# Performance work log

Measured on AMD Instinct MI355X. Metric: run time of the kernel, lower is better.

## Reference

```python
import jax, jax.numpy as jnp
import numpy as np

D_MODEL = 1024
N_HEADS = 16
HEAD_DIM = D_MODEL // N_HEADS
D_FF = 4096
ROPE_BASE = 10000.0
LN_EPS = 1e-5


def setup_inputs() -> dict:
    key = jax.random.key(0)
    ks = jax.random.split(key, 12)
    B, S = 2, 2048
    s = 0.02
    inp = {
        "x": jax.random.normal(ks[0], (B, S, D_MODEL), dtype=jnp.float32),
        "Wq": jax.random.normal(ks[1], (D_MODEL, D_MODEL), dtype=jnp.float32) * s,
        "bq": jnp.zeros((D_MODEL,), jnp.float32),
        "Wk": jax.random.normal(ks[2], (D_MODEL, D_MODEL), dtype=jnp.float32) * s,
        "bk": jnp.zeros((D_MODEL,), jnp.float32),
        "Wv": jax.random.normal(ks[3], (D_MODEL, D_MODEL), dtype=jnp.float32) * s,
        "bv": jnp.zeros((D_MODEL,), jnp.float32),
        "Wo": jax.random.normal(ks[4], (D_MODEL, D_MODEL), dtype=jnp.float32) * s,
        "bo": jnp.zeros((D_MODEL,), jnp.float32),
        "ln1_g": jnp.ones((D_MODEL,), jnp.float32),
        "ln1_b": jnp.zeros((D_MODEL,), jnp.float32),
        "W1": jax.random.normal(ks[5], (D_MODEL, D_FF), dtype=jnp.float32) * s,
        "b1": jnp.zeros((D_FF,), jnp.float32),
        "W2": jax.random.normal(ks[6], (D_FF, D_MODEL), dtype=jnp.float32) * s,
        "b2": jnp.zeros((D_MODEL,), jnp.float32),
        "ln2_g": jnp.ones((D_MODEL,), jnp.float32),
        "ln2_b": jnp.zeros((D_MODEL,), jnp.float32),
    }
    return inp


def _layernorm(x, g, b):
    mu = jnp.mean(x, axis=-1, keepdims=True)
    var = jnp.var(x, axis=-1, keepdims=True)
    return (x - mu) * jax.lax.rsqrt(var + LN_EPS) * g + b


def _rope_cos_sin(seq_len, dtype):
    inv_freq = 1.0 / (ROPE_BASE ** (jnp.arange(0, HEAD_DIM, 2, dtype=jnp.float32) / HEAD_DIM))
    t = jnp.arange(seq_len, dtype=jnp.float32)
    freqs = jnp.einsum("i,j->ij", t, inv_freq)          # [S, HEAD_DIM/2]
    emb = jnp.concatenate([freqs, freqs], axis=-1)        # [S, HEAD_DIM]
    return jnp.cos(emb).astype(dtype), jnp.sin(emb).astype(dtype)


def _rotate_half(x):
    x1, x2 = jnp.split(x, 2, axis=-1)
    return jnp.concatenate([-x2, x1], axis=-1)


def reference(x, Wq, bq, Wk, bk, Wv, bv, Wo, bo, ln1_g, ln1_b,
              W1, b1, W2, b2, ln2_g, ln2_b):
    B, S, _ = x.shape
    residual = x
    h = _layernorm(x, ln1_g, ln1_b)

    def split_heads(y):  # [B,S,D] -> [B,H,S,hd]
        return y.reshape(B, S, N_HEADS, HEAD_DIM).transpose(0, 2, 1, 3)

    q = split_heads(h @ Wq + bq)
    k = split_heads(h @ Wk + bk)
    v = split_heads(h @ Wv + bv)

    cos, sin = _rope_cos_sin(S, x.dtype)  # [S, hd], broadcast over B,H
    q = q * cos + _rotate_half(q) * sin
    k = k * cos + _rotate_half(k) * sin

    scale = HEAD_DIM ** -0.5
    scores = jnp.einsum("bhqd,bhkd->bhqk", q, k) * scale
    attn = jax.nn.softmax(scores, axis=-1)
    ctx = jnp.einsum("bhqk,bhkd->bhqd", attn, v)           # [B,H,S,hd]
    ctx = ctx.transpose(0, 2, 1, 3).reshape(B, S, D_MODEL)
    attn_out = ctx @ Wo + bo

    x = residual + attn_out
    residual = x
    h = _layernorm(x, ln2_g, ln2_b)
    ffn = jax.nn.gelu(h @ W1 + b1, approximate=False) @ W2 + b2
    return residual + ffn
```

## Files before the change

kernel.cpp:

```cpp
#include <hip/hip_runtime.h>
#include <hip/hip_bf16.h>
#include <stdint.h>

#define S_LEN 2048
#define NH 16
#define HD 64
#define DM 1024
#define DFF 4096
#define MTOK 4096

typedef __attribute__((ext_vector_type(8))) short short8;
typedef __attribute__((ext_vector_type(4))) float f32x4;
typedef unsigned short u16;
typedef unsigned int u32;

__device__ __forceinline__ float bf2f(u16 u) {
  union { u32 i; float f; } x; x.i = ((u32)u) << 16; return x.f;
}
__device__ __forceinline__ u16 f2bf(float f) {
  union { float f; u32 i; } x; x.f = f;
  u32 r = x.i + 0x7fffu + ((x.i >> 16) & 1u);
  return (u16)(r >> 16);
}
__device__ __forceinline__ void gload16(const u16* g, u16* l) {
  __builtin_amdgcn_global_load_lds(
      (__attribute__((address_space(1))) u32*)g,
      (__attribute__((address_space(3))) u32*)l, 16, 0, 0);
}

#define VM0 asm volatile("s_waitcnt vmcnt(0)" ::: "memory")
#define VM6 asm volatile("s_waitcnt vmcnt(6)" ::: "memory")
#define BARR do { __builtin_amdgcn_s_barrier(); asm volatile("" ::: "memory"); } while (0)
#define LGKM0 do { asm volatile("s_waitcnt lgkmcnt(0)" ::: "memory"); __builtin_amdgcn_sched_barrier(0); } while (0)
#define PRIO1 __builtin_amdgcn_s_setprio(1)
#define PRIO0 __builtin_amdgcn_s_setprio(0)

__device__ __forceinline__ void transpose_tile(const float* __restrict__ W,
                                               u16* __restrict__ Wt, int K, int N,
                                               int n0, int k0, int tx, int ty,
                                               float (*tile)[33]) {
#pragma unroll
  for (int i = 0; i < 4; ++i)
    tile[ty + i * 8][tx] = W[(size_t)(k0 + ty + i * 8) * N + n0 + tx];
  __syncthreads();
#pragma unroll
  for (int i = 0; i < 4; ++i)
    Wt[(size_t)(n0 + ty + i * 8) * K + k0 + tx] = f2bf(tile[tx][ty + i * 8]);
}

__global__ __launch_bounds__(256) void prep(
    const float* __restrict__ Wq, const float* __restrict__ Wk,
    const float* __restrict__ Wv, const float* __restrict__ Wo,
    const float* __restrict__ W1, const float* __restrict__ W2,
    u16* __restrict__ WQKVT, u16* __restrict__ WOT, u16* __restrict__ W1T,
    u16* __restrict__ W2T, float* __restrict__ cosT, float* __restrict__ sinT,
    const float* __restrict__ x, const float* __restrict__ g,
    const float* __restrict__ b, u16* __restrict__ H) {
  __shared__ float tile[32][33];
  __shared__ float red[8];
  const int r = blockIdx.x;
  const int t = threadIdx.x;
  const int tx = t & 31, ty = t >> 5;
  if (r < 4096) {
    const float* W = (r < 1024) ? Wq : (r < 2048) ? Wk : (r < 3072) ? Wv : Wo;
    u16* Wt = (r < 1024) ? WQKVT
              : (r < 2048) ? WQKVT + 1024 * 1024
              : (r < 3072) ? WQKVT + 2 * 1024 * 1024 : WOT;
    int sub = r & 1023;
    transpose_tile(W, Wt, 1024, 1024, (sub & 31) * 32, (sub >> 5) * 32, tx, ty, tile);
  } else if (r < 8192) {
    int sub = r - 4096;
    transpose_tile(W1, W1T, 1024, 4096, (sub & 127) * 32, (sub >> 7) * 32, tx, ty, tile);
  } else if (r < 12288) {
    int sub = r - 8192;
    transpose_tile(W2, W2T, 4096, 1024, (sub & 31) * 32, (sub >> 5) * 32, tx, ty, tile);
  } else if (r < 12544) {
    int id = (r - 12288) * 256 + t;
    int s = id >> 5, j = id & 31;
    float inv = powf(10000.0f, -(float)j * (1.0f / 32.0f));
    float fr = (float)s * inv;
    cosT[id] = cosf(fr);
    sinT[id] = sinf(fr);
  } else {
    int row = r - 12544;
    float4 v = ((const float4*)(x + ((size_t)row << 10)))[t];
    float s = v.x + v.y + v.z + v.w;
    float q = v.x * v.x + v.y * v.y + v.z * v.z + v.w * v.w;
#pragma unroll
    for (int m = 1; m < 64; m <<= 1) {
      s += __shfl_xor(s, m, 64);
      q += __shfl_xor(q, m, 64);
    }
    int lane = t & 63, w = t >> 6;
    if (lane == 0) { red[w] = s; red[4 + w] = q; }
    __syncthreads();
    s = red[0] + red[1] + red[2] + red[3];
    q = red[4] + red[5] + red[6] + red[7];
    float mu = s * (1.0f / 1024.0f);
    float var = q * (1.0f / 1024.0f) - mu * mu;
    float rstd = rsqrtf(var + 1e-5f);
    float4 gv = ((const float4*)g)[t];
    float4 bv = ((const float4*)b)[t];
    ushort4 o;
    o.x = f2bf((v.x - mu) * rstd * gv.x + bv.x);
    o.y = f2bf((v.y - mu) * rstd * gv.y + bv.y);
    o.z = f2bf((v.z - mu) * rstd * gv.z + bv.z);
    o.w = f2bf((v.w - mu) * rstd * gv.w + bv.w);
    ((ushort4*)(H + ((size_t)row << 10)))[t] = o;
  }
}

__global__ __launch_bounds__(256) void ln_bf16(const float* __restrict__ x,
                                               const float* __restrict__ g,
                                               const float* __restrict__ b,
                                               u16* __restrict__ out) {
  int row = blockIdx.x;
  int t = threadIdx.x;
  float4 v = ((const float4*)(x + ((size_t)row << 10)))[t];
  float s = v.x + v.y + v.z + v.w;
  float q = v.x * v.x + v.y * v.y + v.z * v.z + v.w * v.w;
#pragma unroll
  for (int m = 1; m < 64; m <<= 1) {
    s += __shfl_xor(s, m, 64);
    q += __shfl_xor(q, m, 64);
  }
  __shared__ float red[8];
  int lane = t & 63, w = t >> 6;
  if (lane == 0) { red[w] = s; red[4 + w] = q; }
  __syncthreads();
  s = red[0] + red[1] + red[2] + red[3];
  q = red[4] + red[5] + red[6] + red[7];
  float mu = s * (1.0f / 1024.0f);
  float var = q * (1.0f / 1024.0f) - mu * mu;
  float rstd = rsqrtf(var + 1e-5f);
  float4 gv = ((const float4*)g)[t];
  float4 bv = ((const float4*)b)[t];
  ushort4 o;
  o.x = f2bf((v.x - mu) * rstd * gv.x + bv.x);
  o.y = f2bf((v.y - mu) * rstd * gv.y + bv.y);
  o.z = f2bf((v.z - mu) * rstd * gv.z + bv.z);
  o.w = f2bf((v.w - mu) * rstd * gv.w + bv.w);
  ((ushort4*)(out + ((size_t)row << 10)))[t] = o;
}

#define MMQ(IB, NB)                                                          \
  _Pragma("unroll") for (int i_ = 0; i_ < 4; ++i_)                           \
  _Pragma("unroll") for (int n_ = 0; n_ < 2; ++n_)                           \
  _Pragma("unroll") for (int k_ = 0; k_ < 2; ++k_)                           \
    acc[(IB) + i_][(NB) + n_] = __builtin_amdgcn_mfma_f32_16x16x32_bf16(     \
        a[i_][k_], b[(NB) + n_][k_], acc[(IB) + i_][(NB) + n_], 0, 0, 0);

template <int EPI>
__global__ __launch_bounds__(512, 2) void gemm256(
    const u16* __restrict__ A, const u16* __restrict__ Bt, int N, int K,
    const float* __restrict__ bias, const float* __restrict__ bq,
    const float* __restrict__ bk, const float* __restrict__ bv,
    const float* __restrict__ cosT, const float* __restrict__ sinT,
    u16* __restrict__ d0, u16* __restrict__ d1, u16* __restrict__ d2) {
  __shared__ __align__(16) u16 As[2][256 * 64];
  __shared__ __align__(16) u16 Bs[2][256 * 64];
  const int t = threadIdx.x;
  const int lane = t & 63, wid = t >> 6;
  const int fr = lane & 15, fq = lane >> 4;
  const int m0 = blockIdx.y << 8, n0 = blockIdx.x << 8;
  const int wmo = (wid >> 2) << 7;
  const int wno = (wid & 3) << 6;
  const int r7 = fr & 7;
  const int srow = t >> 3, ssl = t & 7;

  f32x4 acc[8][4];
#pragma unroll
  for (int i = 0; i < 8; ++i)
#pragma unroll
    for (int n = 0; n < 4; ++n) acc[i][n] = (f32x4){0.f, 0.f, 0.f, 0.f};

  short8 a[4][2], b[4][2];

  auto stageA = [&](int slot, int kt) {
#pragma unroll
    for (int c = 0; c < 4; ++c) {
      const int row = (c << 6) + srow;
      gload16(A + (size_t)(m0 + row) * K + kt + ((ssl ^ (row & 7)) << 3),
              &As[slot][(size_t)((c << 9) + t) << 3]);
    }
  };
  auto stageB = [&](int slot, int kt) {
#pragma unroll
    for (int c = 0; c < 4; ++c) {
      const int row = (c << 6) + srow;
      gload16(Bt + (size_t)(n0 + row) * K + kt + ((ssl ^ (row & 7)) << 3),
              &Bs[slot][(size_t)((c << 9) + t) << 3]);
    }
  };
  auto readA = [&](int slot, int ibase) {
#pragma unroll
    for (int i = 0; i < 4; ++i) {
      const u16* rp = &As[slot][(wmo + ((ibase + i) << 4) + fr) << 6];
      a[i][0] = *(const short8*)(rp + ((fq ^ r7) << 3));
      a[i][1] = *(const short8*)(rp + (((4 + fq) ^ r7) << 3));
    }
  };
  auto readB = [&](int slot, int nbase) {
#pragma unroll
    for (int n = 0; n < 2; ++n) {
      const u16* rp = &Bs[slot][(wno + ((nbase + n) << 4) + fr) << 6];
      b[nbase + n][0] = *(const short8*)(rp + ((fq ^ r7) << 3));
      b[nbase + n][1] = *(const short8*)(rp + (((4 + fq) ^ r7) << 3));
    }
  };

  stageA(0, 0);
  stageB(0, 0);
  const int iters = K >> 7;
  for (int it = 0; it < iters; ++it) {
    const int kt = it << 7;
    VM0; BARR;
    readA(0, 0); readB(0, 0);
    stageA(1, kt + 64);
    LGKM0; PRIO1; MMQ(0, 0); PRIO0;
    BARR;
    readB(0, 2);
    stageB(1, kt + 64);
    LGKM0; PRIO1; MMQ(0, 2); PRIO0;
    BARR;
    readA(0, 4);
    LGKM0; PRIO1; MMQ(4, 2); PRIO0;
    BARR;
    PRIO1; MMQ(4, 0); PRIO0;
    VM0; BARR;
    readA(1, 0); readB(1, 0);
    if (it + 1 < iters) stageA(0, kt + 128);
    LGKM0; PRIO1; MMQ(0, 0); PRIO0;
    BARR;
    readB(1, 2);
    if (it + 1 < iters) stageB(0, kt + 128);
    LGKM0; PRIO1; MMQ(0, 2); PRIO0;
    BARR;
    readA(1, 4);
    LGKM0; PRIO1; MMQ(4, 2); PRIO0;
    BARR;
    PRIO1; MMQ(4, 0); PRIO0;
  }

  if (EPI == 0) {
    const int colbase = n0 + wno;
    const int slice = colbase >> 10;
    const int cb = colbase & 1023;
    const int hh = cb >> 6;
    if (slice < 2) {
      const float sc = (slice == 0) ? 0.125f * 1.44269504088896f : 1.0f;
      const float* bb_ = (slice == 0) ? bq : bk;
      u16* dst = (slice == 0) ? d0 : d1;
#pragma unroll
      for (int i = 0; i < 8; ++i) {
        const int row0 = m0 + wmo + (i << 4) + (fq << 2);
#pragma unroll
        for (int n = 0; n < 2; ++n) {
          const int d = n * 16 + fr;
          const float blo = bb_[cb + d];
          const float bhi = bb_[cb + d + 32];
#pragma unroll
          for (int j = 0; j < 4; ++j) {
            const int row = row0 + j;
            const int ss = row & 2047, bb2 = row >> 11;
            const float c = cosT[ss * 32 + d];
            const float sn = sinT[ss * 32 + d];
            const float av = acc[i][n][j] + blo;
            const float bv2 = acc[i][n + 2][j] + bhi;
            const size_t base = ((size_t)((bb2 * 16 + hh) * 2048 + ss)) << 6;
            dst[base + d] = f2bf((av * c - bv2 * sn) * sc);
            dst[base + d + 32] = f2bf((bv2 * c + av * sn) * sc);
          }
        }
      }
    } else {
#pragma unroll
      for (int i = 0; i < 8; ++i) {
        const int row0 = m0 + wmo + (i << 4) + (fq << 2);
#pragma unroll
        for (int n = 0; n < 4; ++n) {
          const int d = n * 16 + fr;
          const float bia = bv[cb + d];
#pragma unroll
          for (int j = 0; j < 4; ++j) {
            const int row = row0 + j;
            const int ss = row & 2047, bb2 = row >> 11;
            d2[((size_t)((bb2 * 16 + hh) * 64 + d)) * 2048 + ss] =
                f2bf(acc[i][n][j] + bia);
          }
        }
      }
    }
  } else {
#pragma unroll
    for (int i = 0; i < 8; ++i) {
      const int row0 = m0 + wmo + (i << 4) + (fq << 2);
#pragma unroll
      for (int n = 0; n < 4; ++n) {
        const int col = n0 + wno + n * 16 + fr;
        const float bia = bias[col];
#pragma unroll
        for (int j = 0; j < 4; ++j) {
          const int row = row0 + j;
          const float v = acc[i][n][j] + bia;
          const float gl = 0.5f * v * (1.0f + erff(v * 0.70710678118f));
          d0[(size_t)row * N + col] = f2bf(gl);
        }
      }
    }
  }
}

__global__ __launch_bounds__(256, 2) void gemm_bt2(
    const u16* __restrict__ A, const u16* __restrict__ Bt, int K,
    const float* __restrict__ bias, const float* __restrict__ resid,
    float* __restrict__ dst) {
  __shared__ __align__(16) u16 As[3][128 * 64];
  __shared__ __align__(16) u16 Bs[3][64 * 64];
  const int t = threadIdx.x, lane = t & 63, wid = t >> 6;
  const int fr = lane & 15, fq = lane >> 4;
  const int bid = blockIdx.x;
  const int xcd = bid & 7, within = bid >> 3;
  const int m0 = (xcd * 4 + (within >> 4)) << 7;
  const int n0 = (within & 15) << 6;
  const int wm = (wid >> 1) << 6;
  const int wn = (wid & 1) << 5;
  const int sr = t >> 3, sl = t & 7;
  const int sw7 = fr & 7;

  f32x4 acc[4][2];
#pragma unroll
  for (int i = 0; i < 4; ++i)
#pragma unroll
    for (int n = 0; n < 2; ++n) acc[i][n] = (f32x4){0.f, 0.f, 0.f, 0.f};

  auto stage = [&](int b, int kt) {
#pragma unroll
    for (int c = 0; c < 4; ++c) {
      int R = c * 32 + sr;
      gload16(A + (size_t)(m0 + R) * K + kt + ((sl ^ (R & 7)) << 3),
              &As[b][R * 64 + sl * 8]);
    }
#pragma unroll
    for (int c = 0; c < 2; ++c) {
      int R = c * 32 + sr;
      gload16(Bt + (size_t)(n0 + R) * K + kt + ((sl ^ (R & 7)) << 3),
              &Bs[b][R * 64 + sl * 8]);
    }
  };

  stage(0, 0);
  stage(1, 64);
  const int iters = K >> 6;
  for (int it = 0; it < iters; ++it) {
    if (it + 1 < iters) { VM6; } else { VM0; }
    BARR;
    if (it + 2 < iters) stage((it + 2) % 3, (it + 2) << 6);
    const int slot = it % 3;
    short8 a[4][2], b[2][2];
#pragma unroll
    for (int i = 0; i < 4; ++i) {
      const char* rp = (const char*)&As[slot][(wm + i * 16 + fr) * 64];
      a[i][0] = *(const short8*)(rp + ((fq ^ sw7) << 4));
      a[i][1] = *(const short8*)(rp + (((4 + fq) ^ sw7) << 4));
    }
#pragma unroll
    for (int n = 0; n < 2; ++n) {
      const char* rp = (const char*)&Bs[slot][(wn + n * 16 + fr) * 64];
      b[n][0] = *(const short8*)(rp + ((fq ^ sw7) << 4));
      b[n][1] = *(const short8*)(rp + (((4 + fq) ^ sw7) << 4));
    }
    PRIO1;
#pragma unroll
    for (int i = 0; i < 4; ++i)
#pragma unroll
      for (int n = 0; n < 2; ++n)
#pragma unroll
        for (int k2 = 0; k2 < 2; ++k2)
          acc[i][n] = __builtin_amdgcn_mfma_f32_16x16x32_bf16(a[i][k2], b[n][k2],
                                                              acc[i][n], 0, 0, 0);
    PRIO0;
  }

#pragma unroll
  for (int i = 0; i < 4; ++i) {
    int row0 = m0 + wm + i * 16 + (fq << 2);
#pragma unroll
    for (int n = 0; n < 2; ++n) {
      int col = n0 + wn + n * 16 + fr;
      float bia = bias[col];
#pragma unroll
      for (int j = 0; j < 4; ++j) {
        size_t idx = (size_t)(row0 + j) * 1024 + col;
        dst[idx] = acc[i][n][j] + bia + resid[idx];
      }
    }
  }
}

__global__ __launch_bounds__(256, 4) void attn_fwd(const u16* __restrict__ q,
                                                   const u16* __restrict__ k,
                                                   const u16* __restrict__ vt,
                                                   u16* __restrict__ ctx) {
  __shared__ __align__(16) u16 Ks[2][64 * 64];
  __shared__ __align__(16) u16 Vs[2][64 * 64];
  __shared__ __align__(16) u16 Pb[4][16 * 64];
  const int t = threadIdx.x, lane = t & 63, w = t >> 6;
  const int fr = lane & 15, fq = lane >> 4;
  const int bid = blockIdx.x;
  const int bh = (bid & 7) * 4 + ((bid >> 3) & 3);
  const int qt = bid >> 5;
  const int q0w = qt * 64 + w * 16;
  const size_t hbase = (size_t)bh << 17;
  const u16* kg = k + hbase;
  const u16* vg = vt + hbase;
  const int sr = t >> 3;
  const int sl = t & 7;
  const int sw7 = fr & 7;

  short8 aq0, aq1;
  {
    const u16* qp = q + hbase + (size_t)(q0w + fr) * 64 + fq * 8;
    aq0 = *(const short8*)qp;
    aq1 = *(const short8*)(qp + 32);
  }

  float mrow = -3e38f, lrow = 0.f;
  f32x4 o[4];
#pragma unroll
  for (int n = 0; n < 4; ++n) o[n] = (f32x4){0.f, 0.f, 0.f, 0.f};

  auto stage = [&](int buf, int kt) {
#pragma unroll
    for (int c = 0; c < 2; ++c) {
      int R = c * 32 + sr;
      int gs = sl ^ (R & 7);
      gload16(kg + (size_t)(kt + R) * 64 + gs * 8, &Ks[buf][R * 64 + sl * 8]);
    }
#pragma unroll
    for (int c = 0; c < 2; ++c) {
      int R = c * 32 + sr;
      int gs = sl ^ (R & 7);
      gload16(vg + (size_t)R * 2048 + kt + gs * 8, &Vs[buf][R * 64 + sl * 8]);
    }
  };

  stage(0, 0);
  int buf = 0;
  for (int it = 0; it < 32; ++it) {
    VM0;
    BARR;
    if (it < 31) stage(buf ^ 1, (it + 1) * 64);

    f32x4 s[4];
    const char* kbase = (const char*)&Ks[buf][0];
    PRIO1;
#pragma unroll
    for (int n = 0; n < 4; ++n) {
      const char* kr = kbase + (n * 16 + fr) * 128;
      short8 kb0 = *(const short8*)(kr + ((fq ^ sw7) << 4));
      short8 kb1 = *(const short8*)(kr + (((4 + fq) ^ sw7) << 4));
      s[n] = (f32x4){0.f, 0.f, 0.f, 0.f};
      s[n] = __builtin_amdgcn_mfma_f32_16x16x32_bf16(kb0, aq0, s[n], 0, 0, 0);
      s[n] = __builtin_amdgcn_mfma_f32_16x16x32_bf16(kb1, aq1, s[n], 0, 0, 0);
    }
    PRIO0;

    float m0 = fmaxf(fmaxf(s[0][0], s[0][1]), fmaxf(s[0][2], s[0][3]));
    float m1 = fmaxf(fmaxf(s[1][0], s[1][1]), fmaxf(s[1][2], s[1][3]));
    float m2 = fmaxf(fmaxf(s[2][0], s[2][1]), fmaxf(s[2][2], s[2][3]));
    float m3 = fmaxf(fmaxf(s[3][0], s[3][1]), fmaxf(s[3][2], s[3][3]));
    float pm = fmaxf(fmaxf(m0, m1), fmaxf(m2, m3));
    pm = fmaxf(pm, __shfl_xor(pm, 16, 64));
    pm = fmaxf(pm, __shfl_xor(pm, 32, 64));

    if (!__all(pm - mrow <= 8.0f)) {
      float mnew = fmaxf(mrow, pm);
      float alpha = exp2f(mrow - mnew);
      mrow = mnew;
      lrow *= alpha;
      float al[4];
#pragma unroll
      for (int j = 0; j < 4; ++j) al[j] = __shfl(alpha, fq * 4 + j, 64);
#pragma unroll
      for (int n = 0; n < 4; ++n)
#pragma unroll
        for (int j = 0; j < 4; ++j) o[n][j] *= al[j];
    }

    float rs = 0.f;
    char* pw = (char*)&Pb[w][0];
#pragma unroll
    for (int n = 0; n < 4; ++n) {
#pragma unroll
      for (int jp = 0; jp < 2; ++jp) {
        float p0 = exp2f(s[n][2 * jp] - mrow);
        float p1 = exp2f(s[n][2 * jp + 1] - mrow);
        rs += p0 + p1;
        union { float f; u32 i; } u0, u1;
        u0.f = p0; u1.f = p1;
        u32 pk = (u0.i >> 16) | (u1.i & 0xffff0000u);
        int off = fr * 128 + ((n * 32 + fq * 8 + jp * 4) ^ (sw7 << 4));
        *(u32*)(pw + off) = pk;
      }
    }
    rs += __shfl_xor(rs, 16, 64);
    rs += __shfl_xor(rs, 32, 64);
    lrow += rs;

    LGKM0;
    const char* prd = (const char*)&Pb[w][0];
    short8 ap0 = *(const short8*)(prd + fr * 128 + ((fq ^ sw7) << 4));
    short8 ap1 = *(const short8*)(prd + fr * 128 + (((4 + fq) ^ sw7) << 4));

    const char* vbase = (const char*)&Vs[buf][0];
    PRIO1;
#pragma unroll
    for (int n = 0; n < 4; ++n) {
      const char* vr = vbase + (n * 16 + fr) * 128;
      short8 vb0 = *(const short8*)(vr + ((fq ^ sw7) << 4));
      short8 vb1 = *(const short8*)(vr + (((4 + fq) ^ sw7) << 4));
      o[n] = __builtin_amdgcn_mfma_f32_16x16x32_bf16(ap0, vb0, o[n], 0, 0, 0);
      o[n] = __builtin_amdgcn_mfma_f32_16x16x32_bf16(ap1, vb1, o[n], 0, 0, 0);
    }
    PRIO0;
    buf ^= 1;
  }

  const int bb = bh >> 4, hh = bh & 15;
  float rl[4];
#pragma unroll
  for (int j = 0; j < 4; ++j) rl[j] = 1.0f / __shfl(lrow, fq * 4 + j, 64);
#pragma unroll
  for (int n = 0; n < 4; ++n) {
    int d = n * 16 + fr;
#pragma unroll
    for (int j = 0; j < 4; ++j) {
      int row = q0w + fq * 4 + j;
      ctx[(((size_t)(bb * 2048 + row)) << 10) + hh * 64 + d] = f2bf(o[n][j] * rl[j]);
    }
  }
}

extern "C" void kernel_launch(void* const* d_in, const int* in_sizes, int n_in,
                              void* d_out, int out_size, void* d_ws, size_t ws_size,
                              hipStream_t stream) {
  const float* x    = (const float*)d_in[0];
  const float* Wq   = (const float*)d_in[1];
  const float* bq   = (const float*)d_in[2];
  const float* Wk   = (const float*)d_in[3];
  const float* bk   = (const float*)d_in[4];
  const float* Wv   = (const float*)d_in[5];
  const float* bv   = (const float*)d_in[6];
  const float* Wo   = (const float*)d_in[7];
  const float* bo   = (const float*)d_in[8];
  const float* ln1g = (const float*)d_in[9];
  const float* ln1b = (const float*)d_in[10];
  const float* W1   = (const float*)d_in[11];
  const float* b1   = (const float*)d_in[12];
  const float* W2   = (const float*)d_in[13];
  const float* b2   = (const float*)d_in[14];
  const float* ln2g = (const float*)d_in[15];
  const float* ln2b = (const float*)d_in[16];

  char* ws = (char*)d_ws;
  size_t off = 0;
  auto alloc = [&](size_t bytes) {
    char* p = ws + off;
    off += (bytes + 1023) & ~(size_t)1023;
    return p;
  };
  u16* WQKVT = (u16*)alloc((size_t)3 * DM * DM * 2);
  u16* WOT = (u16*)alloc((size_t)DM * DM * 2);
  u16* W1T = (u16*)alloc((size_t)DFF * DM * 2);
  u16* W2T = (u16*)alloc((size_t)DM * DFF * 2);
  float* COS = (float*)alloc((size_t)S_LEN * 32 * 4);
  float* SIN = (float*)alloc((size_t)S_LEN * 32 * 4);
  u16* H   = (u16*)alloc((size_t)MTOK * DM * 2);
  u16* Qb  = (u16*)alloc((size_t)MTOK * DM * 2);
  u16* Kb  = (u16*)alloc((size_t)MTOK * DM * 2);
  u16* VT  = (u16*)alloc((size_t)MTOK * DM * 2);
  u16* CTX = (u16*)alloc((size_t)MTOK * DM * 2);
  float* X2 = (float*)alloc((size_t)MTOK * DM * 4);
  u16* FFN1 = Qb;
  if (ws_size < off) return;

  dim3 blk256(256);
  prep<<<dim3(16640), blk256, 0, stream>>>(Wq, Wk, Wv, Wo, W1, W2, WQKVT, WOT,
                                           W1T, W2T, COS, SIN, x, ln1g, ln1b, H);
  gemm256<0><<<dim3(12, 16), dim3(512), 0, stream>>>(
      H, WQKVT, 3072, 1024, nullptr, bq, bk, bv, COS, SIN, Qb, Kb, VT);
  attn_fwd<<<dim3(1024), blk256, 0, stream>>>(Qb, Kb, VT, CTX);
  gemm_bt2<<<dim3(512), blk256, 0, stream>>>(CTX, WOT, 1024, bo, x, X2);
  ln_bf16<<<4096, blk256, 0, stream>>>(X2, ln2g, ln2b, H);
  gemm256<1><<<dim3(16, 16), dim3(512), 0, stream>>>(
      H, W1T, 4096, 1024, b1, nullptr, nullptr, nullptr, nullptr, nullptr,
      FFN1, nullptr, nullptr);
  gemm_bt2<<<dim3(512), blk256, 0, stream>>>(FFN1, W2T, 4096, b2, X2, (float*)d_out);
}
```

Measured before the change: 260.1 us.

## Process two query fragments per wave in attention to reuse K/V tiles

Each wave in the attention kernel now handles 32 query rows (two 16-row fragments) instead of 16. Each block covers 128 queries, so the grid halves. K and V fragments read from LDS are reused across both query fragments, which halves K/V global staging and LDS reads per query. P is packed with the v_cvt_pk_bf16_f32 instruction and written as 8-byte stores. The cost is more registers (launch bounds lowered from 4 to 2 blocks per SM), fewer blocks (512) and therefore less occupancy, and conversion switches from truncation to round-to-nearest.

```diff
diff --git a/kernel.cpp b/kernel.cpp
--- a/kernel.cpp
+++ b/kernel.cpp
@@ -398,19 +398,19 @@
   }
 }
 
-__global__ __launch_bounds__(256, 4) void attn_fwd(const u16* __restrict__ q,
+__global__ __launch_bounds__(256, 2) void attn_fwd(const u16* __restrict__ q,
                                                    const u16* __restrict__ k,
                                                    const u16* __restrict__ vt,
                                                    u16* __restrict__ ctx) {
   __shared__ __align__(16) u16 Ks[2][64 * 64];
   __shared__ __align__(16) u16 Vs[2][64 * 64];
-  __shared__ __align__(16) u16 Pb[4][16 * 64];
+  __shared__ __align__(16) u16 Pb[4][2][16 * 64];
   const int t = threadIdx.x, lane = t & 63, w = t >> 6;
   const int fr = lane & 15, fq = lane >> 4;
   const int bid = blockIdx.x;
   const int bh = (bid & 7) * 4 + ((bid >> 3) & 3);
   const int qt = bid >> 5;
-  const int q0w = qt * 64 + w * 16;
+  const int q0w = qt * 128 + w * 32;
   const size_t hbase = (size_t)bh << 17;
   const u16* kg = k + hbase;
   const u16* vg = vt + hbase;
@@ -418,17 +418,20 @@
   const int sl = t & 7;
   const int sw7 = fr & 7;
 
-  short8 aq0, aq1;
-  {
-    const u16* qp = q + hbase + (size_t)(q0w + fr) * 64 + fq * 8;
-    aq0 = *(const short8*)qp;
-    aq1 = *(const short8*)(qp + 32);
-  }
-
-  float mrow = -3e38f, lrow = 0.f;
-  f32x4 o[4];
-#pragma unroll
-  for (int n = 0; n < 4; ++n) o[n] = (f32x4){0.f, 0.f, 0.f, 0.f};
+  short8 aq[2][2];
+#pragma unroll
+  for (int qf = 0; qf < 2; ++qf) {
+    const u16* qp = q + hbase + (size_t)(q0w + qf * 16 + fr) * 64 + fq * 8;
+    aq[qf][0] = *(const short8*)qp;
+    aq[qf][1] = *(const short8*)(qp + 32);
+  }
+
+  float mrow[2] = {-3e38f, -3e38f}, lrow[2] = {0.f, 0.f};
+  f32x4 o[2][4];
+#pragma unroll
+  for (int qf = 0; qf < 2; ++qf)
+#pragma unroll
+    for (int n = 0; n < 4; ++n) o[qf][n] = (f32x4){0.f, 0.f, 0.f, 0.f};
 
   auto stage = [&](int buf, int kt) {
 #pragma unroll
@@ -452,66 +455,86 @@
     BARR;
     if (it < 31) stage(buf ^ 1, (it + 1) * 64);
 
-    f32x4 s[4];
+    short8 kb[4][2];
     const char* kbase = (const char*)&Ks[buf][0];
-    PRIO1;
 #pragma unroll
     for (int n = 0; n < 4; ++n) {
       const char* kr = kbase + (n * 16 + fr) * 128;
-      short8 kb0 = *(const short8*)(kr + ((fq ^ sw7) << 4));
-      short8 kb1 = *(const short8*)(kr + (((4 + fq) ^ sw7) << 4));
-      s[n] = (f32x4){0.f, 0.f, 0.f, 0.f};
-      s[n] = __builtin_amdgcn_mfma_f32_16x16x32_bf16(kb0, aq0, s[n], 0, 0, 0);
-      s[n] = __builtin_amdgcn_mfma_f32_16x16x32_bf16(kb1, aq1, s[n], 0, 0, 0);
-    }
+      kb[n][0] = *(const short8*)(kr + ((fq ^ sw7) << 4));
+      kb[n][1] = *(const short8*)(kr + (((4 + fq) ^ sw7) << 4));
+    }
+    f32x4 s[2][4];
+    PRIO1;
+#pragma unroll
+    for (int qf = 0; qf < 2; ++qf)
+#pragma unroll
+      for (int n = 0; n < 4; ++n) {
+        s[qf][n] = (f32x4){0.f, 0.f, 0.f, 0.f};
+        s[qf][n] = __builtin_amdgcn_mfma_f32_16x16x32_bf16(kb[n][0], aq[qf][0], s[qf][n], 0, 0, 0);
+        s[qf][n] = __builtin_amdgcn_mfma_f32_16x16x32_bf16(kb[n][1], aq[qf][1], s[qf][n], 0, 0, 0);
+      }
     PRIO0;
 
-    float m0 = fmaxf(fmaxf(s[0][0], s[0][1]), fmaxf(s[0][2], s[0][3]));
-    float m1 = fmaxf(fmaxf(s[1][0], s[1][1]), fmaxf(s[1][2], s[1][3]));
-    float m2 = fmaxf(fmaxf(s[2][0], s[2][1]), fmaxf(s[2][2], s[2][3]));
-    float m3 = fmaxf(fmaxf(s[3][0], s[3][1]), fmaxf(s[3][2], s[3][3]));
-    float pm = fmaxf(fmaxf(m0, m1), fmaxf(m2, m3));
-    pm = fmaxf(pm, __shfl_xor(pm, 16, 64));
-    pm = fmaxf(pm, __shfl_xor(pm, 32, 64));
-
-    if (!__all(pm - mrow <= 8.0f)) {
-      float mnew = fmaxf(mrow, pm);
-      float alpha = exp2f(mrow - mnew);
-      mrow = mnew;
-      lrow *= alpha;
-      float al[4];
-#pragma unroll
-      for (int j = 0; j < 4; ++j) al[j] = __shfl(alpha, fq * 4 + j, 64);
-#pragma unroll
-      for (int n = 0; n < 4; ++n)
-#pragma unroll
-        for (int j = 0; j < 4; ++j) o[n][j] *= al[j];
-    }
-
-    float rs = 0.f;
-    char* pw = (char*)&Pb[w][0];
-#pragma unroll
-    for (int n = 0; n < 4; ++n) {
-#pragma unroll
-      for (int jp = 0; jp < 2; ++jp) {
-        float p0 = exp2f(s[n][2 * jp] - mrow);
-        float p1 = exp2f(s[n][2 * jp + 1] - mrow);
-        rs += p0 + p1;
-        union { float f; u32 i; } u0, u1;
-        u0.f = p0; u1.f = p1;
-        u32 pk = (u0.i >> 16) | (u1.i & 0xffff0000u);
-        int off = fr * 128 + ((n * 32 + fq * 8 + jp * 4) ^ (sw7 << 4));
-        *(u32*)(pw + off) = pk;
-      }
-    }
-    rs += __shfl_xor(rs, 16, 64);
-    rs += __shfl_xor(rs, 32, 64);
-    lrow += rs;
+    float pm[2];
+#pragma unroll
+    for (int qf = 0; qf < 2; ++qf) {
+      float a0 = fmaxf(fmaxf(s[qf][0][0], s[qf][0][1]), fmaxf(s[qf][0][2], s[qf][0][3]));
+      float a1 = fmaxf(fmaxf(s[qf][1][0], s[qf][1][1]), fmaxf(s[qf][1][2], s[qf][1][3]));
+      float a2 = fmaxf(fmaxf(s[qf][2][0], s[qf][2][1]), fmaxf(s[qf][2][2], s[qf][2][3]));
+      float a3 = fmaxf(fmaxf(s[qf][3][0], s[qf][3][1]), fmaxf(s[qf][3][2], s[qf][3][3]));
+      float m = fmaxf(fmaxf(a0, a1), fmaxf(a2, a3));
+      m = fmaxf(m, __shfl_xor(m, 16, 64));
+      m = fmaxf(m, __shfl_xor(m, 32, 64));
+      pm[qf] = m;
+    }
+
+    if (!__all(fmaxf(pm[0] - mrow[0], pm[1] - mrow[1]) <= 8.0f)) {
+#pragma unroll
+      for (int qf = 0; qf < 2; ++qf) {
+        float mnew = fmaxf(mrow[qf], pm[qf]);
+        float alpha = exp2f(mrow[qf] - mnew);
+        mrow[qf] = mnew;
+        lrow[qf] *= alpha;
+        float al[4];
+#pragma unroll
+        for (int j = 0; j < 4; ++j) al[j] = __shfl(alpha, fq * 4 + j, 64);
+#pragma unroll
+        for (int n = 0; n < 4; ++n)
+#pragma unroll
+          for (int j = 0; j < 4; ++j) o[qf][n][j] *= al[j];
+      }
+    }
+
+#pragma unroll
+    for (int qf = 0; qf < 2; ++qf) {
+      float rs = 0.f;
+      char* pw = (char*)&Pb[w][qf][0];
+#pragma unroll
+      for (int n = 0; n < 4; ++n) {
+        float p0 = exp2f(s[qf][n][0] - mrow[qf]);
+        float p1 = exp2f(s[qf][n][1] - mrow[qf]);
+        float p2 = exp2f(s[qf][n][2] - mrow[qf]);
+        float p3 = exp2f(s[qf][n][3] - mrow[qf]);
+        rs += (p0 + p1) + (p2 + p3);
+        u32 d0, d1;
+        asm volatile("v_cvt_pk_bf16_f32 %0, %1, %2" : "=v"(d0) : "v"(p0), "v"(p1));
+        asm volatile("v_cvt_pk_bf16_f32 %0, %1, %2" : "=v"(d1) : "v"(p2), "v"(p3));
+        int off = fr * 128 + ((n * 32 + fq * 8) ^ (sw7 << 4));
+        *(uint2*)(pw + off) = make_uint2(d0, d1);
+      }
+      rs += __shfl_xor(rs, 16, 64);
+      rs += __shfl_xor(rs, 32, 64);
+      lrow[qf] += rs;
+    }
 
     LGKM0;
-    const char* prd = (const char*)&Pb[w][0];
-    short8 ap0 = *(const short8*)(prd + fr * 128 + ((fq ^ sw7) << 4));
-    short8 ap1 = *(const short8*)(prd + fr * 128 + (((4 + fq) ^ sw7) << 4));
+    short8 ap[2][2];
+#pragma unroll
+    for (int qf = 0; qf < 2; ++qf) {
+      const char* prd = (const char*)&Pb[w][qf][0];
+      ap[qf][0] = *(const short8*)(prd + fr * 128 + ((fq ^ sw7) << 4));
+      ap[qf][1] = *(const short8*)(prd + fr * 128 + (((4 + fq) ^ sw7) << 4));
+    }
 
     const char* vbase = (const char*)&Vs[buf][0];
     PRIO1;
@@ -520,24 +543,29 @@
       const char* vr = vbase + (n * 16 + fr) * 128;
       short8 vb0 = *(const short8*)(vr + ((fq ^ sw7) << 4));
       short8 vb1 = *(const short8*)(vr + (((4 + fq) ^ sw7) << 4));
-      o[n] = __builtin_amdgcn_mfma_f32_16x16x32_bf16(ap0, vb0, o[n], 0, 0, 0);
-      o[n] = __builtin_amdgcn_mfma_f32_16x16x32_bf16(ap1, vb1, o[n], 0, 0, 0);
+      o[0][n] = __builtin_amdgcn_mfma_f32_16x16x32_bf16(ap[0][0], vb0, o[0][n], 0, 0, 0);
+      o[0][n] = __builtin_amdgcn_mfma_f32_16x16x32_bf16(ap[0][1], vb1, o[0][n], 0, 0, 0);
+      o[1][n] = __builtin_amdgcn_mfma_f32_16x16x32_bf16(ap[1][0], vb0, o[1][n], 0, 0, 0);
+      o[1][n] = __builtin_amdgcn_mfma_f32_16x16x32_bf16(ap[1][1], vb1, o[1][n], 0, 0, 0);
     }
     PRIO0;
     buf ^= 1;
   }
 
   const int bb = bh >> 4, hh = bh & 15;
-  float rl[4];
-#pragma unroll
-  for (int j = 0; j < 4; ++j) rl[j] = 1.0f / __shfl(lrow, fq * 4 + j, 64);
-#pragma unroll
-  for (int n = 0; n < 4; ++n) {
-    int d = n * 16 + fr;
-#pragma unroll
-    for (int j = 0; j < 4; ++j) {
-      int row = q0w + fq * 4 + j;
-      ctx[(((size_t)(bb * 2048 + row)) << 10) + hh * 64 + d] = f2bf(o[n][j] * rl[j]);
+#pragma unroll
+  for (int qf = 0; qf < 2; ++qf) {
+    float rl[4];
+#pragma unroll
+    for (int j = 0; j < 4; ++j) rl[j] = 1.0f / __shfl(lrow[qf], fq * 4 + j, 64);
+#pragma unroll
+    for (int n = 0; n < 4; ++n) {
+      int d = n * 16 + fr;
+#pragma unroll
+      for (int j = 0; j < 4; ++j) {
+        int row = q0w + qf * 16 + fq * 4 + j;
+        ctx[(((size_t)(bb * 2048 + row)) << 10) + hh * 64 + d] = f2bf(o[qf][n][j] * rl[j]);
+      }
     }
   }
 }
@@ -590,7 +618,7 @@
                                            W1T, W2T, COS, SIN, x, ln1g, ln1b, H);
   gemm256<0><<<dim3(12, 16), dim3(512), 0, stream>>>(
       H, WQKVT, 3072, 1024, nullptr, bq, bk, bv, COS, SIN, Qb, Kb, VT);
-  attn_fwd<<<dim3(1024), blk256, 0, stream>>>(Qb, Kb, VT, CTX);
+  attn_fwd<<<dim3(512), blk256, 0, stream>>>(Qb, Kb, VT, CTX);
   gemm_bt2<<<dim3(512), blk256, 0, stream>>>(CTX, WOT, 1024, bo, x, X2);
   ln_bf16<<<4096, blk256, 0, stream>>>(X2, ln2g, ln2b, H);
   gemm256<1><<<dim3(16, 16), dim3(512), 0, stream>>>(
```

Result: no change. 257.7 us (-1.0%).

## Double attention query tile per block to 8 waves and pack P with cvt_pk_bf16

Applied to the files above, without the earlier changes.

The attention kernel now runs 512 threads (8 waves) per block, and each block covers 128 query rows instead of 64. Each staged K/V tile is therefore shared by twice as many waves, which halves global K/V traffic and per-block staging work; each thread now issues one load per tile. The softmax probability packing replaces manual truncating bit-packing with the hardware v_cvt_pk_bf16_f32 instruction and one 64-bit LDS store per fragment. The trade-offs are half as many blocks (512) and a different register budget under the new launch bounds, which could reduce occupancy or latency hiding. The conversion also changes from truncation to rounding.

```diff
diff --git a/kernel.cpp b/kernel.cpp
--- a/kernel.cpp
+++ b/kernel.cpp
@@ -398,19 +398,19 @@
   }
 }
 
-__global__ __launch_bounds__(256, 4) void attn_fwd(const u16* __restrict__ q,
+__global__ __launch_bounds__(512, 4) void attn_fwd(const u16* __restrict__ q,
                                                    const u16* __restrict__ k,
                                                    const u16* __restrict__ vt,
                                                    u16* __restrict__ ctx) {
   __shared__ __align__(16) u16 Ks[2][64 * 64];
   __shared__ __align__(16) u16 Vs[2][64 * 64];
-  __shared__ __align__(16) u16 Pb[4][16 * 64];
+  __shared__ __align__(16) u16 Pb[8][16 * 64];
   const int t = threadIdx.x, lane = t & 63, w = t >> 6;
   const int fr = lane & 15, fq = lane >> 4;
   const int bid = blockIdx.x;
   const int bh = (bid & 7) * 4 + ((bid >> 3) & 3);
   const int qt = bid >> 5;
-  const int q0w = qt * 64 + w * 16;
+  const int q0w = qt * 128 + w * 16;
   const size_t hbase = (size_t)bh << 17;
   const u16* kg = k + hbase;
   const u16* vg = vt + hbase;
@@ -431,18 +431,9 @@
   for (int n = 0; n < 4; ++n) o[n] = (f32x4){0.f, 0.f, 0.f, 0.f};
 
   auto stage = [&](int buf, int kt) {
-#pragma unroll
-    for (int c = 0; c < 2; ++c) {
-      int R = c * 32 + sr;
-      int gs = sl ^ (R & 7);
-      gload16(kg + (size_t)(kt + R) * 64 + gs * 8, &Ks[buf][R * 64 + sl * 8]);
-    }
-#pragma unroll
-    for (int c = 0; c < 2; ++c) {
-      int R = c * 32 + sr;
-      int gs = sl ^ (R & 7);
-      gload16(vg + (size_t)R * 2048 + kt + gs * 8, &Vs[buf][R * 64 + sl * 8]);
-    }
+    int gs = sl ^ (sr & 7);
+    gload16(kg + (size_t)(kt + sr) * 64 + gs * 8, &Ks[buf][sr * 64 + sl * 8]);
+    gload16(vg + (size_t)sr * 2048 + kt + gs * 8, &Vs[buf][sr * 64 + sl * 8]);
   };
 
   stage(0, 0);
@@ -492,17 +483,16 @@
     char* pw = (char*)&Pb[w][0];
 #pragma unroll
     for (int n = 0; n < 4; ++n) {
-#pragma unroll
-      for (int jp = 0; jp < 2; ++jp) {
-        float p0 = exp2f(s[n][2 * jp] - mrow);
-        float p1 = exp2f(s[n][2 * jp + 1] - mrow);
-        rs += p0 + p1;
-        union { float f; u32 i; } u0, u1;
-        u0.f = p0; u1.f = p1;
-        u32 pk = (u0.i >> 16) | (u1.i & 0xffff0000u);
-        int off = fr * 128 + ((n * 32 + fq * 8 + jp * 4) ^ (sw7 << 4));
-        *(u32*)(pw + off) = pk;
-      }
+      float p0 = exp2f(s[n][0] - mrow);
+      float p1 = exp2f(s[n][1] - mrow);
+      float p2 = exp2f(s[n][2] - mrow);
+      float p3 = exp2f(s[n][3] - mrow);
+      rs += (p0 + p1) + (p2 + p3);
+      u32 d0, d1;
+      asm volatile("v_cvt_pk_bf16_f32 %0, %1, %2" : "=v"(d0) : "v"(p0), "v"(p1));
+      asm volatile("v_cvt_pk_bf16_f32 %0, %1, %2" : "=v"(d1) : "v"(p2), "v"(p3));
+      int off = fr * 128 + ((n * 32 + fq * 8) ^ (sw7 << 4));
+      *(uint2*)(pw + off) = make_uint2(d0, d1);
     }
     rs += __shfl_xor(rs, 16, 64);
     rs += __shfl_xor(rs, 32, 64);
@@ -590,7 +580,7 @@
                                            W1T, W2T, COS, SIN, x, ln1g, ln1b, H);
   gemm256<0><<<dim3(12, 16), dim3(512), 0, stream>>>(
       H, WQKVT, 3072, 1024, nullptr, bq, bk, bv, COS, SIN, Qb, Kb, VT);
-  attn_fwd<<<dim3(1024), blk256, 0, stream>>>(Qb, Kb, VT, CTX);
+  attn_fwd<<<dim3(512), dim3(512), 0, stream>>>(Qb, Kb, VT, CTX);
   gemm_bt2<<<dim3(512), blk256, 0, stream>>>(CTX, WOT, 1024, bo, x, X2);
   ln_bf16<<<4096, blk256, 0, stream>>>(X2, ln2g, ln2b, H);
   gemm256<1><<<dim3(16, 16), dim3(512), 0, stream>>>(
```

Result: faster. 253.2 us (-2.7%).
